# Kernel tuning notes

Hardware: AMD Instinct MI355X
Metric: run time of the kernel (lower is better)

## Reference

```python
import jax, jax.numpy as jnp
import numpy as np

TEMP = 0.07
NEG_INF = -1e30  # finite stand-in for -inf; safe under vjp


def setup_inputs() -> dict:
    key = jax.random.key(0)
    k1, k2, k3 = jax.random.split(key, 3)
    B, D, H, F = 16384, 2048, 2048, 128  # 2N rows, backbone_dim, hidden_dim, feature_dim
    features = jax.random.normal(k1, (B, D), dtype=jnp.float32)
    w1 = jax.random.normal(k2, (D, H), dtype=jnp.float32) / np.sqrt(D)
    b1 = jnp.zeros((H,), dtype=jnp.float32)
    w2 = jax.random.normal(k3, (H, F), dtype=jnp.float32) / np.sqrt(H)
    b2 = jnp.zeros((F,), dtype=jnp.float32)
    return {"features": features, "w1": w1, "b1": b1, "w2": w2, "b2": b2}


def reference(features, w1, b1, w2, b2):
    # Projector: Linear -> ReLU -> Linear, then L2-normalize (F.normalize, dim=1)
    h = jax.nn.relu(features @ w1 + b1)
    p = h @ w2 + b2
    z = p / jnp.maximum(jnp.linalg.norm(p, axis=1, keepdims=True), 1e-12)

    M = z.shape[0]           # 2N
    N = M // 2
    sim = (z @ z.T) / TEMP   # [2N, 2N]

    # NT-Xent with labels=0: loss_i = logsumexp_{j != i}(sim[i,j]) - pos_i
    # (pos appears exactly once among the logits, so the gather loop over
    #  per-row negatives collapses to a diagonal-masked row logsumexp).
    diag = jnp.eye(M, dtype=bool)
    lse = jax.nn.logsumexp(jnp.where(diag, NEG_INF, sim), axis=1)
    pos = jnp.sum(z * jnp.roll(z, N, axis=0), axis=1) / TEMP  # sim[i, (i+N) % 2N]
    loss = jnp.mean(lse - pos)
    return loss, z[:N], z[N:]
```

## Files before the change

kernel.cpp:

```cpp
#include <hip/hip_runtime.h>

typedef __attribute__((ext_vector_type(8))) __bf16 bf16x8;
typedef __attribute__((ext_vector_type(4))) float f32x4;

#define B_ROWS 16384
#define N_HALF 8192
#define D_DIM  2048
#define H_DIM  2048
#define F_DIM  128

static constexpr float kInvT = 14.285714285714286f;
static constexpr float kS2   = 20.60992915555662f;

__device__ __forceinline__ void async16(void* lds, const void* g) {
  __builtin_amdgcn_global_load_lds((const __attribute__((address_space(1))) void*)g,
                                   (__attribute__((address_space(3))) void*)lds,
                                   16, 0, 0);
}

__global__ void cvt_bf16_kernel(const float* __restrict__ in, __bf16* __restrict__ out, int n) {
  int i = (blockIdx.x * blockDim.x + threadIdx.x) * 8;
  if (i >= n) return;
  float4 a = *(const float4*)(in + i);
  float4 b = *(const float4*)(in + i + 4);
  bf16x8 o;
  o[0] = (__bf16)a.x; o[1] = (__bf16)a.y; o[2] = (__bf16)a.z; o[3] = (__bf16)a.w;
  o[4] = (__bf16)b.x; o[5] = (__bf16)b.y; o[6] = (__bf16)b.z; o[7] = (__bf16)b.w;
  *(bf16x8*)(out + i) = o;
}

__global__ void transpose_cvt_kernel(const float* __restrict__ in, __bf16* __restrict__ out,
                                     int R, int C) {
  __shared__ float tile[32][33];
  int tx = threadIdx.x, ty = threadIdx.y;
  int c0 = blockIdx.x * 32, r0 = blockIdx.y * 32;
  for (int i = 0; i < 4; i++)
    tile[ty + i * 8][tx] = in[(size_t)(r0 + ty + i * 8) * C + c0 + tx];
  __syncthreads();
  for (int i = 0; i < 4; i++)
    out[(size_t)(c0 + ty + i * 8) * R + r0 + tx] = (__bf16)tile[tx][ty + i * 8];
}

#define BM 256
#define BK 64
#define NT_K (D_DIM / BK)

__global__ __launch_bounds__(512, 2) void gemm1_8ph_kernel(
    const __bf16* __restrict__ A, const __bf16* __restrict__ BT,
    const float* __restrict__ bias, __bf16* __restrict__ C) {
  __shared__ __align__(16) __bf16 As[2][BM * BK];
  __shared__ __align__(16) __bf16 Bs[2][BM * BK];
  const int t = threadIdx.x;
  const int wave = t >> 6, lane = t & 63;
  const int l15 = lane & 15, quad = lane >> 4, l7 = l15 & 7;
  const int wy = wave & 1, wx = wave >> 1;

  const int wg = ((int)blockIdx.x & 7) * 64 + ((int)blockIdx.x >> 3);
  const int n0 = (wg & 7) * 256;
  const int m0 = (wg >> 3) * 256;

  const int tr = t >> 3;
  const int csw = ((t & 7) ^ (tr & 7)) * 8;
  const __bf16* pA = A + (size_t)(m0 + tr) * D_DIM + csw;
  const __bf16* pB = BT + (size_t)(n0 + tr) * D_DIM + csw;
  const int ldsw = wave * 512;

  auto stageA = [&](int buf, int h, int kk) {
    async16(&As[buf][h * 8192 + ldsw], pA + (size_t)(h * 128) * D_DIM + kk);
    async16(&As[buf][h * 8192 + 4096 + ldsw], pA + (size_t)(h * 128 + 64) * D_DIM + kk);
  };
  auto stageB = [&](int buf, int h, int kk) {
    async16(&Bs[buf][h * 8192 + ldsw], pB + (size_t)(h * 128) * D_DIM + kk);
    async16(&Bs[buf][h * 8192 + 4096 + ldsw], pB + (size_t)(h * 128 + 64) * D_DIM + kk);
  };

  const int arow = wy * 16 + l15;
  const int brow = wx * 16 + l15;
  const int s0 = (quad ^ l7) * 8;
  const int s1 = ((4 + quad) ^ l7) * 8;

  f32x4 acc[8][4];
#pragma unroll
  for (int f = 0; f < 8; f++)
#pragma unroll
    for (int n = 0; n < 4; n++) acc[f][n] = 0.f;

  stageB(0, 0, 0); stageB(0, 1, 0);
  stageA(0, 0, 0); stageA(0, 1, 0);
  stageB(1, 0, BK); stageB(1, 1, BK);
  asm volatile("s_waitcnt vmcnt(4)" ::: "memory");
  __builtin_amdgcn_s_barrier();

  for (int tk = 0; tk < NT_K; ++tk) {
    const int cur = tk & 1, nxt = cur ^ 1;
    const __bf16* Ac = &As[cur][0];
    const __bf16* Bc = &Bs[cur][0];
#define LDA(f, s) (*(const bf16x8*)(Ac + ((f) * 32 + arow) * 64 + (s)))
#define LDB(n, s) (*(const bf16x8*)(Bc + ((n) * 64 + brow) * 64 + (s)))
    bf16x8 b0[4], b1[4];
    {
      bf16x8 a0 = LDA(0, s0), a1 = LDA(1, s0), a2 = LDA(2, s0), a3 = LDA(3, s0);
      b0[0] = LDB(0, s0); b0[1] = LDB(1, s0); b0[2] = LDB(2, s0); b0[3] = LDB(3, s0);
      if (tk + 1 < NT_K) stageA(nxt, 0, (tk + 1) * BK);
      __builtin_amdgcn_s_barrier();
      asm volatile("s_waitcnt lgkmcnt(0)" ::: "memory");
      __builtin_amdgcn_s_setprio(1);
#pragma unroll
      for (int n = 0; n < 4; n++) {
        acc[0][n] = __builtin_amdgcn_mfma_f32_16x16x32_bf16(a0, b0[n], acc[0][n], 0, 0, 0);
        acc[1][n] = __builtin_amdgcn_mfma_f32_16x16x32_bf16(a1, b0[n], acc[1][n], 0, 0, 0);
        acc[2][n] = __builtin_amdgcn_mfma_f32_16x16x32_bf16(a2, b0[n], acc[2][n], 0, 0, 0);
        acc[3][n] = __builtin_amdgcn_mfma_f32_16x16x32_bf16(a3, b0[n], acc[3][n], 0, 0, 0);
      }
      __builtin_amdgcn_s_setprio(0);
      __builtin_amdgcn_s_barrier();
    }
    {
      bf16x8 a4 = LDA(4, s0), a5 = LDA(5, s0), a6 = LDA(6, s0), a7 = LDA(7, s0);
      if (tk + 1 < NT_K) stageA(nxt, 1, (tk + 1) * BK);
      __builtin_amdgcn_s_barrier();
      asm volatile("s_waitcnt lgkmcnt(0)" ::: "memory");
      __builtin_amdgcn_s_setprio(1);
#pragma unroll
      for (int n = 0; n < 4; n++) {
        acc[4][n] = __builtin_amdgcn_mfma_f32_16x16x32_bf16(a4, b0[n], acc[4][n], 0, 0, 0);
        acc[5][n] = __builtin_amdgcn_mfma_f32_16x16x32_bf16(a5, b0[n], acc[5][n], 0, 0, 0);
        acc[6][n] = __builtin_amdgcn_mfma_f32_16x16x32_bf16(a6, b0[n], acc[6][n], 0, 0, 0);
        acc[7][n] = __builtin_amdgcn_mfma_f32_16x16x32_bf16(a7, b0[n], acc[7][n], 0, 0, 0);
      }
      __builtin_amdgcn_s_setprio(0);
      __builtin_amdgcn_s_barrier();
    }
    {
      bf16x8 a0 = LDA(0, s1), a1 = LDA(1, s1), a2 = LDA(2, s1), a3 = LDA(3, s1);
      b1[0] = LDB(0, s1); b1[1] = LDB(1, s1); b1[2] = LDB(2, s1); b1[3] = LDB(3, s1);
      __builtin_amdgcn_s_barrier();
      asm volatile("s_waitcnt lgkmcnt(0)" ::: "memory");
      __builtin_amdgcn_s_setprio(1);
#pragma unroll
      for (int n = 0; n < 4; n++) {
        acc[0][n] = __builtin_amdgcn_mfma_f32_16x16x32_bf16(a0, b1[n], acc[0][n], 0, 0, 0);
        acc[1][n] = __builtin_amdgcn_mfma_f32_16x16x32_bf16(a1, b1[n], acc[1][n], 0, 0, 0);
        acc[2][n] = __builtin_amdgcn_mfma_f32_16x16x32_bf16(a2, b1[n], acc[2][n], 0, 0, 0);
        acc[3][n] = __builtin_amdgcn_mfma_f32_16x16x32_bf16(a3, b1[n], acc[3][n], 0, 0, 0);
      }
      __builtin_amdgcn_s_setprio(0);
      __builtin_amdgcn_s_barrier();
    }
    {
      bf16x8 a4 = LDA(4, s1), a5 = LDA(5, s1), a6 = LDA(6, s1), a7 = LDA(7, s1);
      const bool st = (tk + 2 < NT_K);
      if (st) {
        stageB(cur, 0, (tk + 2) * BK);
        stageB(cur, 1, (tk + 2) * BK);
      }
      __builtin_amdgcn_s_barrier();
      asm volatile("s_waitcnt lgkmcnt(0)" ::: "memory");
      __builtin_amdgcn_s_setprio(1);
#pragma unroll
      for (int n = 0; n < 4; n++) {
        acc[4][n] = __builtin_amdgcn_mfma_f32_16x16x32_bf16(a4, b1[n], acc[4][n], 0, 0, 0);
        acc[5][n] = __builtin_amdgcn_mfma_f32_16x16x32_bf16(a5, b1[n], acc[5][n], 0, 0, 0);
        acc[6][n] = __builtin_amdgcn_mfma_f32_16x16x32_bf16(a6, b1[n], acc[6][n], 0, 0, 0);
        acc[7][n] = __builtin_amdgcn_mfma_f32_16x16x32_bf16(a7, b1[n], acc[7][n], 0, 0, 0);
      }
      __builtin_amdgcn_s_setprio(0);
      if (st) {
        asm volatile("s_waitcnt vmcnt(4)" ::: "memory");
      } else if (tk + 1 < NT_K) {
        asm volatile("s_waitcnt vmcnt(0)" ::: "memory");
      }
      __builtin_amdgcn_s_barrier();
    }
#undef LDA
#undef LDB
  }

#pragma unroll
  for (int n = 0; n < 4; n++) {
    int col = n0 + n * 64 + wx * 16 + l15;
    float bv = bias[col];
#pragma unroll
    for (int f = 0; f < 8; f++) {
      int rowb = m0 + f * 32 + wy * 16 + quad * 4;
#pragma unroll
      for (int r = 0; r < 4; r++) {
        float v = fmaxf(acc[f][n][r] + bv, 0.f);
        C[(size_t)(rowb + r) * H_DIM + col] = (__bf16)v;
      }
    }
  }
}

__global__ __launch_bounds__(256) void proj_norm_kernel(
    const __bf16* __restrict__ A, const __bf16* __restrict__ BT,
    const float* __restrict__ bias, float* __restrict__ zf, __bf16* __restrict__ zb, int K) {
  __shared__ __align__(16) __bf16 As[5 * 64 * 32];
  __shared__ __align__(16) __bf16 Bs[5 * 128 * 32];
  __shared__ float pbuf[64 * 128];
  const int t = threadIdx.x;
  const int wave = t >> 6, lane = t & 63;
  const int l15 = lane & 15, quad = lane >> 4;
  const int wy = wave >> 1, wx = wave & 1;
  const int m0 = blockIdx.x * 64;
  const int sr = t >> 2;
  const int sk = (((t & 3) ^ ((sr >> 1) & 3))) * 8;
  const int sw = (l15 >> 1) & 3;
  const int NK = K / 32;

  auto stage = [&](int buf, int k0) {
    async16(As + buf * 2048 + wave * 512, A + (size_t)(m0 + sr) * K + k0 + sk);
    async16(Bs + buf * 4096 + wave * 512, BT + (size_t)(0  + sr) * K + k0 + sk);
    async16(Bs + buf * 4096 + 2048 + wave * 512, BT + (size_t)(64 + sr) * K + k0 + sk);
  };

  f32x4 acc[2][4];
  for (int i = 0; i < 2; i++)
    for (int j = 0; j < 4; j++) acc[i][j] = 0.f;

  stage(0, 0); stage(1, 32); stage(2, 64); stage(3, 96);
  asm volatile("s_waitcnt vmcnt(9)" ::: "memory");
  __builtin_amdgcn_s_barrier();

  for (int kk = 0; kk < NK; ++kk) {
    const int cur = kk % 5;
    bf16x8 af[2], bfr[4];
    for (int i = 0; i < 2; i++)
      af[i] = *(const bf16x8*)(As + cur * 2048 + (wy * 32 + i * 16 + l15) * 32 + (quad ^ sw) * 8);
    for (int i = 0; i < 4; i++)
      bfr[i] = *(const bf16x8*)(Bs + cur * 4096 + (wx * 64 + i * 16 + l15) * 32 + (quad ^ sw) * 8);
    if (kk + 4 < NK) stage((kk + 4) % 5, (kk + 4) * 32);
    asm volatile("s_waitcnt lgkmcnt(0)" ::: "memory");
    if (kk + 4 < NK) {
      asm volatile("s_waitcnt vmcnt(9)" ::: "memory");
    } else if (kk == NK - 4) {
      asm volatile("s_waitcnt vmcnt(6)" ::: "memory");
    } else if (kk == NK - 3) {
      asm volatile("s_waitcnt vmcnt(3)" ::: "memory");
    } else {
      asm volatile("s_waitcnt vmcnt(0)" ::: "memory");
    }
    __builtin_amdgcn_s_barrier();
    for (int mi = 0; mi < 2; mi++)
      for (int ni = 0; ni < 4; ni++)
        acc[mi][ni] = __builtin_amdgcn_mfma_f32_16x16x32_bf16(af[mi], bfr[ni], acc[mi][ni], 0, 0, 0);
  }
  __syncthreads();
  for (int ni = 0; ni < 4; ni++) {
    int col = wx * 64 + ni * 16 + l15;
    float bv = bias[col];
    for (int mi = 0; mi < 2; mi++) {
      int lrow = wy * 32 + mi * 16 + quad * 4;
      for (int r = 0; r < 4; r++)
        pbuf[(lrow + r) * 128 + col] = acc[mi][ni][r] + bv;
    }
  }
  __syncthreads();
  for (int it = 0; it < 16; it++) {
    int lrow = wave * 16 + it;
    float v0 = pbuf[lrow * 128 + lane];
    float v1 = pbuf[lrow * 128 + 64 + lane];
    float ss = v0 * v0 + v1 * v1;
    for (int m = 1; m < 64; m <<= 1) ss += __shfl_xor(ss, m);
    float inv = 1.f / fmaxf(sqrtf(ss), 1e-12f);
    float z0 = v0 * inv, z1 = v1 * inv;
    size_t base = (size_t)(m0 + lrow) * F_DIM;
    zf[base + lane] = z0;
    zf[base + 64 + lane] = z1;
    zb[base + lane] = (__bf16)z0;
    zb[base + 64 + lane] = (__bf16)z1;
  }
}

__global__ __launch_bounds__(256) void sim_lse_tri_kernel(const __bf16* __restrict__ zb,
                                                          float* __restrict__ S,
                                                          float* __restrict__ colpart) {
  __shared__ __align__(16) __bf16 Bs[128 * 128];
  const int t = threadIdx.x;
  const int wave = t >> 6, lane = t & 63;
  const int l15 = lane & 15, quad = lane >> 4;
  const int wy = wave >> 1, wx = wave & 1;
  const int srow = t >> 4;
  const int schunk = (t & 15) ^ srow;

  const int u0 = (int)(((long)blockIdx.x * 8256) >> 10);
  const int u1 = (int)(((long)(blockIdx.x + 1) * 8256) >> 10);

  auto fr = [](int r) { return r * 128 - (r * (r - 1)) / 2; };
  int rt = (int)(128.5f - sqrtf(16512.25f - 2.0f * (float)u0));
  while (fr(rt + 1) <= u0) rt++;
  while (fr(rt) > u0) rt--;
  int ct = rt + (u0 - fr(rt));

  bf16x8 a[4][4];
  float rowacc[4][4];
  auto load_a = [&](int rtile) {
#pragma unroll
    for (int mi = 0; mi < 4; mi++)
#pragma unroll
      for (int ks = 0; ks < 4; ks++)
        a[mi][ks] = *(const bf16x8*)(zb + (size_t)(rtile * 128 + wy * 64 + mi * 16 + l15) * 128 +
                                     ks * 32 + quad * 8);
  };
  auto flush_rows = [&](int rtile) {
#pragma unroll
    for (int mi = 0; mi < 4; mi++)
#pragma unroll
      for (int r = 0; r < 4; r++) {
        float v = rowacc[mi][r];
        v += __shfl_xor(v, 1);
        v += __shfl_xor(v, 2);
        v += __shfl_xor(v, 4);
        v += __shfl_xor(v, 8);
        if (l15 == 0)
          atomicAdd(&S[rtile * 128 + wy * 64 + mi * 16 + quad * 4 + r], v);
        rowacc[mi][r] = 0.f;
      }
  };

#pragma unroll
  for (int mi = 0; mi < 4; mi++)
#pragma unroll
    for (int r = 0; r < 4; r++) rowacc[mi][r] = 0.f;
  load_a(rt);

  for (int u = u0; u < u1; ++u) {
    const __bf16* gbase = zb + (size_t)(ct * 128) * 128;
#pragma unroll
    for (int q = 0; q < 8; q++)
      async16(Bs + q * 2048 + wave * 512, gbase + (size_t)(q * 16 + srow) * 128 + schunk * 8);
    __syncthreads();
    const bool diag = (ct == rt);
#pragma unroll
    for (int ni = 0; ni < 4; ni++) {
      bf16x8 b[4];
      const int brow = wx * 64 + ni * 16 + l15;
#pragma unroll
      for (int ks = 0; ks < 4; ks++)
        b[ks] = *(const bf16x8*)(Bs + brow * 128 + (((ks * 4 + quad) ^ l15) * 8));
      float colsum = 0.f;
      if (diag) {
#pragma unroll
        for (int mi = 0; mi < 4; mi++) {
          f32x4 acc = 0.f;
#pragma unroll
          for (int ks = 0; ks < 4; ks++)
            acc = __builtin_amdgcn_mfma_f32_16x16x32_bf16(a[mi][ks], b[ks], acc, 0, 0, 0);
          const int lrb = wy * 64 + mi * 16 + quad * 4;
#pragma unroll
          for (int r = 0; r < 4; r++) {
            float term = __builtin_amdgcn_exp2f(fmaf(acc[r], kS2, -kS2));
            rowacc[mi][r] += (lrb + r == brow) ? 0.f : term;
          }
        }
      } else {
#pragma unroll
        for (int mi = 0; mi < 4; mi++) {
          f32x4 acc = 0.f;
#pragma unroll
          for (int ks = 0; ks < 4; ks++)
            acc = __builtin_amdgcn_mfma_f32_16x16x32_bf16(a[mi][ks], b[ks], acc, 0, 0, 0);
#pragma unroll
          for (int r = 0; r < 4; r++) {
            float term = __builtin_amdgcn_exp2f(fmaf(acc[r], kS2, -kS2));
            rowacc[mi][r] += term;
            colsum += term;
          }
        }
        colsum += __shfl_xor(colsum, 16);
        colsum += __shfl_xor(colsum, 32);
        if (quad == 0)
          colpart[((size_t)(ct * 128 + rt) * 2 + wy) * 128 + brow] = colsum;
      }
    }
    __syncthreads();
    if (u + 1 < u1) {
      ct++;
      if (ct == 128) {
        flush_rows(rt);
        rt++;
        ct = rt;
        load_a(rt);
      }
    }
  }
  flush_rows(rt);
}

__global__ __launch_bounds__(128) void col_reduce_kernel(const float* __restrict__ colpart,
                                                         float* __restrict__ S) {
  const int ct = blockIdx.y;
  const int r0 = blockIdx.x * 32;
  if (r0 >= ct) return;
  const int t = threadIdx.x;
  const int rend = min(ct, r0 + 32);
  float s = 0.f;
  for (int rt = r0; rt < rend; rt++) {
    const float* p = colpart + (size_t)(ct * 128 + rt) * 2 * 128;
    s += p[t] + p[128 + t];
  }
  atomicAdd(&S[ct * 128 + t], s);
}

__global__ void loss_kernel(const float* __restrict__ zf, const float* __restrict__ S,
                            float* __restrict__ out) {
  int wave = threadIdx.x >> 6, lane = threadIdx.x & 63;
  int base = blockIdx.x * 64 + wave * 16;
  float local = 0.f;
  for (int it = 0; it < 16; it++) {
    int row = base + it;
    int j = (row + N_HALF) & (B_ROWS - 1);
    const float* za = zf + (size_t)row * F_DIM;
    const float* zc = zf + (size_t)j * F_DIM;
    float d = za[lane] * zc[lane] + za[lane + 64] * zc[lane + 64];
    for (int m = 1; m < 64; m <<= 1) d += __shfl_xor(d, m);
    float pos = d * kInvT;
    float lse = logf(S[row]) + kInvT;
    local += (lse - pos);
  }
  if (lane == 0) atomicAdd(out, local * (1.f / B_ROWS));
}

extern "C" void kernel_launch(void* const* d_in, const int* in_sizes, int n_in,
                              void* d_out, int out_size, void* d_ws, size_t ws_size,
                              hipStream_t stream) {
  const float* features = (const float*)d_in[0];
  const float* w1 = (const float*)d_in[1];
  const float* b1 = (const float*)d_in[2];
  const float* w2 = (const float*)d_in[3];
  const float* b2 = (const float*)d_in[4];
  float* out = (float*)d_out;

  char* ws = (char*)d_ws;
  size_t off = 0;
  __bf16* A1  = (__bf16*)(ws + off); off += (size_t)B_ROWS * D_DIM * 2;
  __bf16* h   = (__bf16*)(ws + off); off += (size_t)B_ROWS * H_DIM * 2;
  __bf16* w1t = (__bf16*)(ws + off); off += (size_t)H_DIM * D_DIM * 2;
  __bf16* w2t = (__bf16*)(ws + off); off += (size_t)F_DIM * H_DIM * 2;
  __bf16* zbb = (__bf16*)(ws + off); off += (size_t)B_ROWS * F_DIM * 2;
  float*  S   = (float*)(ws + off);  off += (size_t)B_ROWS * 4;
  float* colpart = (float*)A1;

  hipMemsetAsync(S, 0, (size_t)B_ROWS * 4, stream);
  hipMemsetAsync(out, 0, 4, stream);

  {
    int n = B_ROWS * D_DIM;
    cvt_bf16_kernel<<<n / (256 * 8), 256, 0, stream>>>(features, A1, n);
  }
  transpose_cvt_kernel<<<dim3(H_DIM / 32, D_DIM / 32), dim3(32, 8), 0, stream>>>(w1, w1t, D_DIM, H_DIM);
  transpose_cvt_kernel<<<dim3(F_DIM / 32, H_DIM / 32), dim3(32, 8), 0, stream>>>(w2, w2t, H_DIM, F_DIM);

  gemm1_8ph_kernel<<<dim3((B_ROWS / 256) * (H_DIM / 256)), 512, 0, stream>>>(A1, w1t, b1, h);

  proj_norm_kernel<<<B_ROWS / 64, 256, 0, stream>>>(h, w2t, b2, out + 1, zbb, H_DIM);

  sim_lse_tri_kernel<<<1024, 256, 0, stream>>>(zbb, S, colpart);
  col_reduce_kernel<<<dim3(4, 128), 128, 0, stream>>>(colpart, S);

  loss_kernel<<<B_ROWS / 64, 256, 0, stream>>>(out + 1, S, out);
}
```

Before: 482.3 us.

## Fuse fp32-to-bf16 feature conversion into GEMM1 A-tile loading

```diff
diff --git a/kernel.cpp b/kernel.cpp
--- a/kernel.cpp
+++ b/kernel.cpp
@@ -18,15 +18,11 @@
                                    16, 0, 0);
 }
 
-__global__ void cvt_bf16_kernel(const float* __restrict__ in, __bf16* __restrict__ out, int n) {
-  int i = (blockIdx.x * blockDim.x + threadIdx.x) * 8;
-  if (i >= n) return;
-  float4 a = *(const float4*)(in + i);
-  float4 b = *(const float4*)(in + i + 4);
+__device__ __forceinline__ void write8(__bf16* d, float4 a, float4 b) {
   bf16x8 o;
   o[0] = (__bf16)a.x; o[1] = (__bf16)a.y; o[2] = (__bf16)a.z; o[3] = (__bf16)a.w;
   o[4] = (__bf16)b.x; o[5] = (__bf16)b.y; o[6] = (__bf16)b.z; o[7] = (__bf16)b.w;
-  *(bf16x8*)(out + i) = o;
+  *(bf16x8*)d = o;
 }
 
 __global__ void transpose_cvt_kernel(const float* __restrict__ in, __bf16* __restrict__ out,
@@ -46,7 +42,7 @@
 #define NT_K (D_DIM / BK)
 
 __global__ __launch_bounds__(512, 2) void gemm1_8ph_kernel(
-    const __bf16* __restrict__ A, const __bf16* __restrict__ BT,
+    const float* __restrict__ Af, const __bf16* __restrict__ BT,
     const float* __restrict__ bias, __bf16* __restrict__ C) {
   __shared__ __align__(16) __bf16 As[2][BM * BK];
   __shared__ __align__(16) __bf16 Bs[2][BM * BK];
@@ -61,17 +57,27 @@
 
   const int tr = t >> 3;
   const int csw = ((t & 7) ^ (tr & 7)) * 8;
-  const __bf16* pA = A + (size_t)(m0 + tr) * D_DIM + csw;
+  const float* pAf = Af + (size_t)(m0 + tr) * D_DIM + csw;
   const __bf16* pB = BT + (size_t)(n0 + tr) * D_DIM + csw;
   const int ldsw = wave * 512;
 
-  auto stageA = [&](int buf, int h, int kk) {
-    async16(&As[buf][h * 8192 + ldsw], pA + (size_t)(h * 128) * D_DIM + kk);
-    async16(&As[buf][h * 8192 + 4096 + ldsw], pA + (size_t)(h * 128 + 64) * D_DIM + kk);
-  };
   auto stageB = [&](int buf, int h, int kk) {
     async16(&Bs[buf][h * 8192 + ldsw], pB + (size_t)(h * 128) * D_DIM + kk);
     async16(&Bs[buf][h * 8192 + 4096 + ldsw], pB + (size_t)(h * 128 + 64) * D_DIM + kk);
+  };
+  auto loadA = [&](int kk, float4* f) {
+    const float* p0 = pAf + kk;
+#pragma unroll
+    for (int g = 0; g < 4; g++) {
+      f[2 * g]     = *(const float4*)(p0 + (size_t)(g * 64) * D_DIM);
+      f[2 * g + 1] = *(const float4*)(p0 + (size_t)(g * 64) * D_DIM + 4);
+    }
+  };
+  auto writeA = [&](int buf, const float4* f) {
+    write8(&As[buf][0 * 8192 + t * 8],        f[0], f[1]);
+    write8(&As[buf][0 * 8192 + 4096 + t * 8], f[2], f[3]);
+    write8(&As[buf][1 * 8192 + t * 8],        f[4], f[5]);
+    write8(&As[buf][1 * 8192 + 4096 + t * 8], f[6], f[7]);
   };
 
   const int arow = wy * 16 + l15;
@@ -85,10 +91,16 @@
 #pragma unroll
     for (int n = 0; n < 4; n++) acc[f][n] = 0.f;
 
-  stageB(0, 0, 0); stageB(0, 1, 0);
-  stageA(0, 0, 0); stageA(0, 1, 0);
-  stageB(1, 0, BK); stageB(1, 1, BK);
-  asm volatile("s_waitcnt vmcnt(4)" ::: "memory");
+  {
+    float4 f0[8];
+    loadA(0, f0);
+    stageB(0, 0, 0); stageB(0, 1, 0);
+    stageB(1, 0, BK); stageB(1, 1, BK);
+    asm volatile("s_waitcnt vmcnt(8)" ::: "memory");
+    writeA(0, f0);
+    asm volatile("s_waitcnt lgkmcnt(0)" ::: "memory");
+    asm volatile("s_waitcnt vmcnt(4)" ::: "memory");
+  }
   __builtin_amdgcn_s_barrier();
 
   for (int tk = 0; tk < NT_K; ++tk) {
@@ -98,10 +110,11 @@
 #define LDA(f, s) (*(const bf16x8*)(Ac + ((f) * 32 + arow) * 64 + (s)))
 #define LDB(n, s) (*(const bf16x8*)(Bc + ((n) * 64 + brow) * 64 + (s)))
     bf16x8 b0[4], b1[4];
+    float4 fA[8];
+    const bool stA = (tk + 1 < NT_K);
     {
       bf16x8 a0 = LDA(0, s0), a1 = LDA(1, s0), a2 = LDA(2, s0), a3 = LDA(3, s0);
       b0[0] = LDB(0, s0); b0[1] = LDB(1, s0); b0[2] = LDB(2, s0); b0[3] = LDB(3, s0);
-      if (tk + 1 < NT_K) stageA(nxt, 0, (tk + 1) * BK);
       __builtin_amdgcn_s_barrier();
       asm volatile("s_waitcnt lgkmcnt(0)" ::: "memory");
       __builtin_amdgcn_s_setprio(1);
@@ -117,7 +130,6 @@
     }
     {
       bf16x8 a4 = LDA(4, s0), a5 = LDA(5, s0), a6 = LDA(6, s0), a7 = LDA(7, s0);
-      if (tk + 1 < NT_K) stageA(nxt, 1, (tk + 1) * BK);
       __builtin_amdgcn_s_barrier();
       asm volatile("s_waitcnt lgkmcnt(0)" ::: "memory");
       __builtin_amdgcn_s_setprio(1);
@@ -132,6 +144,7 @@
       __builtin_amdgcn_s_barrier();
     }
     {
+      if (stA) loadA((tk + 1) * BK, fA);
       bf16x8 a0 = LDA(0, s1), a1 = LDA(1, s1), a2 = LDA(2, s1), a3 = LDA(3, s1);
       b1[0] = LDB(0, s1); b1[1] = LDB(1, s1); b1[2] = LDB(2, s1); b1[3] = LDB(3, s1);
       __builtin_amdgcn_s_barrier();
@@ -165,10 +178,14 @@
         acc[7][n] = __builtin_amdgcn_mfma_f32_16x16x32_bf16(a7, b1[n], acc[7][n], 0, 0, 0);
       }
       __builtin_amdgcn_s_setprio(0);
-      if (st) {
-        asm volatile("s_waitcnt vmcnt(4)" ::: "memory");
-      } else if (tk + 1 < NT_K) {
-        asm volatile("s_waitcnt vmcnt(0)" ::: "memory");
+      if (stA) {
+        if (st) {
+          asm volatile("s_waitcnt vmcnt(4)" ::: "memory");
+        } else {
+          asm volatile("s_waitcnt vmcnt(0)" ::: "memory");
+        }
+        writeA(nxt, fA);
+        asm volatile("s_waitcnt lgkmcnt(0)" ::: "memory");
       }
       __builtin_amdgcn_s_barrier();
     }
@@ -444,14 +461,10 @@
   hipMemsetAsync(S, 0, (size_t)B_ROWS * 4, stream);
   hipMemsetAsync(out, 0, 4, stream);
 
-  {
-    int n = B_ROWS * D_DIM;
-    cvt_bf16_kernel<<<n / (256 * 8), 256, 0, stream>>>(features, A1, n);
-  }
   transpose_cvt_kernel<<<dim3(H_DIM / 32, D_DIM / 32), dim3(32, 8), 0, stream>>>(w1, w1t, D_DIM, H_DIM);
   transpose_cvt_kernel<<<dim3(F_DIM / 32, H_DIM / 32), dim3(32, 8), 0, stream>>>(w2, w2t, H_DIM, F_DIM);
 
-  gemm1_8ph_kernel<<<dim3((B_ROWS / 256) * (H_DIM / 256)), 512, 0, stream>>>(A1, w1t, b1, h);
+  gemm1_8ph_kernel<<<dim3((B_ROWS / 256) * (H_DIM / 256)), 512, 0, stream>>>(features, w1t, b1, h);
 
   proj_norm_kernel<<<B_ROWS / 64, 256, 0, stream>>>(h, w2t, b2, out + 1, zbb, H_DIM);
 
```

After: 512.7 us. 1.06x slower.
